# Performance work log

Hardware: AMD Instinct MI355X
Metric: run time of the kernel (lower is better)

## Reference

```python
import jax, jax.numpy as jnp
import numpy as np

B, T, D, H = 2, 2048, 1024, 16
DH = D // H

def setup_inputs() -> dict:
    key = jax.random.key(0)
    ks = jax.random.split(key, 5)
    scale = 1.0 / np.sqrt(D)
    x = jax.random.normal(ks[0], (B, T, D), dtype=jnp.float32)
    Wq = jax.random.normal(ks[1], (D, D), dtype=jnp.float32) * scale
    Wk = jax.random.normal(ks[2], (D, D), dtype=jnp.float32) * scale
    Wv = jax.random.normal(ks[3], (D, D), dtype=jnp.float32) * scale
    Wo = jax.random.normal(ks[4], (D, D), dtype=jnp.float32) * scale
    # causal mask: True means masked (matches torch masked_fill semantics)
    mask = jnp.triu(jnp.ones((T, T), dtype=bool), k=1)
    return {"x": x, "mask": mask, "Wq": Wq, "Wk": Wk, "Wv": Wv, "Wo": Wo}

def reference(x, mask, Wq, Wk, Wv, Wo):
    b, t, c = x.shape
    # projections -> [B, H, T, DH]
    def split_heads(y):
        return y.reshape(b, t, H, DH).transpose(0, 2, 1, 3)
    q = split_heads(x @ Wq)
    k = split_heads(x @ Wk)
    v = split_heads(x @ Wv)
    # scores [B, H, T, T]
    att = jnp.einsum('bhqd,bhkd->bhqk', q, k) / jnp.sqrt(jnp.float32(DH))
    att = jnp.where(mask, -jnp.inf, att)
    att = jax.nn.softmax(att, axis=-1)
    # dropout=0.0 (eval-mode determinism)
    out = jnp.einsum('bhqk,bhkd->bhqd', att, v)
    out = out.transpose(0, 2, 1, 3).reshape(b, t, c)
    return out @ Wo
```

## Files before the change

kernel.cpp:

```cpp
#include <hip/hip_runtime.h>
#include <stdint.h>

typedef unsigned short u16;
typedef unsigned int u32;
typedef __attribute__((ext_vector_type(8))) short s16x8;
typedef __attribute__((ext_vector_type(4))) float f32x4;
typedef __attribute__((ext_vector_type(8))) unsigned short u16x8;
typedef __attribute__((ext_vector_type(4))) unsigned short u16x4;

#define T_ 2048
#define D_ 1024
#define H_ 16
#define DH_ 64

#define QSCALE_LOG2E 0.18033688011112042f

#if __has_builtin(__builtin_amdgcn_exp2f)
#define EXP2(x) __builtin_amdgcn_exp2f(x)
#else
#define EXP2(x) exp2f(x)
#endif

__device__ __forceinline__ float bf2f(u16 u) {
    union { unsigned int i; float f; } x; x.i = ((unsigned int)u) << 16; return x.f;
}
__device__ __forceinline__ u16 f2bf(float f) {
    union { float f; unsigned int i; } x; x.f = f;
    unsigned int u = x.i;
    u += 0x7fffu + ((u >> 16) & 1u);
    return (u16)(u >> 16);
}
__device__ __forceinline__ u32 pack_rn(float a, float b) {
    union { float f; u32 u; } ua, ub; ua.f = a; ub.f = b;
    return ((ua.u + 0x8000u) >> 16) | ((ub.u + 0x8000u) & 0xffff0000u);
}

__device__ __forceinline__ void gload16(const u16* g, u16* l) {
    __builtin_amdgcn_global_load_lds(
        (const __attribute__((address_space(1))) void*)g,
        (__attribute__((address_space(3))) void*)l,
        16, 0, 0);
}

__global__ __launch_bounds__(256) void prep_kernel(const float* __restrict__ x,
                                                   const float* __restrict__ Wq,
                                                   const float* __restrict__ Wk,
                                                   const float* __restrict__ Wv,
                                                   const float* __restrict__ Wo,
                                                   u16* __restrict__ xb,
                                                   u16* __restrict__ WT) {
    __shared__ float tile[32][33];
    int blk = blockIdx.x;
    if (blk < 4096) {
        int i = (blk * 256 + threadIdx.x) * 4;
        float4 v = *(const float4*)(x + i);
        u16x4 o;
        o[0] = f2bf(v.x); o[1] = f2bf(v.y); o[2] = f2bf(v.z); o[3] = f2bf(v.w);
        *(u16x4*)(xb + i) = o;
    } else {
        int t = blk - 4096;
        int s = t >> 10;
        const float* W = (s == 0) ? Wq : (s == 1) ? Wk : (s == 2) ? Wv : Wo;
        int n0 = ((t >> 5) & 31) * 32;
        int k0 = (t & 31) * 32;
        int tx = threadIdx.x & 31, ty = threadIdx.x >> 5;
        #pragma unroll
        for (int j = 0; j < 32; j += 8)
            tile[ty + j][tx] = W[(k0 + ty + j) * D_ + n0 + tx];
        __syncthreads();
        u16* dst = WT + (size_t)s * D_ * D_;
        #pragma unroll
        for (int j = 0; j < 32; j += 8)
            dst[(n0 + ty + j) * D_ + k0 + tx] = f2bf(tile[tx][ty + j]);
    }
}

__global__ __launch_bounds__(256) void gemm_qkv(const u16* __restrict__ A,
                                                const u16* __restrict__ Bt,
                                                u16* __restrict__ Qw,
                                                u16* __restrict__ Kw,
                                                u16* __restrict__ Vw) {
    __shared__ __align__(16) u16 As[2][128 * 32];
    __shared__ __align__(16) u16 Bs[2][128 * 32];
    const int m0 = blockIdx.x * 128, n0 = blockIdx.y * 128;
    int tid = threadIdx.x;
    int w = tid >> 6, lane = tid & 63, quad = lane >> 4, l15 = lane & 15;
    int wr = w >> 1, wc = w & 1;

    int nb0 = (w << 7), nb1 = nb0 + 64;
    int c0 = nb0 + lane, c1 = nb1 + lane;
    int r0 = c0 >> 2, k0off = (((c0 & 3) ^ ((r0 >> 1) & 3)) << 3);
    int r1 = c1 >> 2, k1off = (((c1 & 3) ^ ((r1 >> 1) & 3)) << 3);
    const u16* Ar0 = A + (size_t)(m0 + r0) * D_ + k0off;
    const u16* Ar1 = A + (size_t)(m0 + r1) * D_ + k1off;
    const u16* Br0 = Bt + (size_t)(n0 + r0) * D_ + k0off;
    const u16* Br1 = Bt + (size_t)(n0 + r1) * D_ + k1off;

    f32x4 acc[4][4];
    #pragma unroll
    for (int mi = 0; mi < 4; ++mi)
        #pragma unroll
        for (int ni = 0; ni < 4; ++ni) acc[mi][ni] = (f32x4){0.f, 0.f, 0.f, 0.f};

    gload16(Ar0, &As[0][nb0 << 3]);
    gload16(Ar1, &As[0][nb1 << 3]);
    gload16(Br0, &Bs[0][nb0 << 3]);
    gload16(Br1, &Bs[0][nb1 << 3]);

    for (int k0 = 0; k0 < D_; k0 += 32) {
        int buf = (k0 >> 5) & 1;
        __syncthreads();
        if (k0 + 32 < D_) {
            int kn = k0 + 32;
            gload16(Ar0 + kn, &As[buf ^ 1][nb0 << 3]);
            gload16(Ar1 + kn, &As[buf ^ 1][nb1 << 3]);
            gload16(Br0 + kn, &Bs[buf ^ 1][nb0 << 3]);
            gload16(Br1 + kn, &Bs[buf ^ 1][nb1 << 3]);
        }
        s16x8 af[4], bf[4];
        #pragma unroll
        for (int mi = 0; mi < 4; ++mi) {
            int R = wr * 64 + mi * 16 + l15;
            af[mi] = *(const s16x8*)&As[buf][((R << 2) | (quad ^ ((R >> 1) & 3))) << 3];
        }
        #pragma unroll
        for (int ni = 0; ni < 4; ++ni) {
            int R = wc * 64 + ni * 16 + l15;
            bf[ni] = *(const s16x8*)&Bs[buf][((R << 2) | (quad ^ ((R >> 1) & 3))) << 3];
        }
        #pragma unroll
        for (int mi = 0; mi < 4; ++mi)
            #pragma unroll
            for (int ni = 0; ni < 4; ++ni)
                acc[mi][ni] = __builtin_amdgcn_mfma_f32_16x16x32_bf16(af[mi], bf[ni],
                                                                      acc[mi][ni], 0, 0, 0);
    }

    #pragma unroll
    for (int mi = 0; mi < 4; ++mi) {
        int mbase = m0 + wr * 64 + mi * 16 + quad * 4;
        #pragma unroll
        for (int ni = 0; ni < 4; ++ni) {
            int n = n0 + wc * 64 + ni * 16 + l15;
            int b = mbase >> 11, t0 = mbase & 2047;
            int sel = n >> 10, nn = n & 1023;
            int h = nn >> 6, dh = nn & 63;
            int bhidx = (b << 4) + h;
            if (sel == 0) {
                #pragma unroll
                for (int r = 0; r < 4; ++r)
                    Qw[(size_t)(bhidx * T_ + t0 + r) * DH_ + dh] =
                        f2bf(acc[mi][ni][r] * QSCALE_LOG2E);
            } else if (sel == 1) {
                #pragma unroll
                for (int r = 0; r < 4; ++r)
                    Kw[(size_t)(bhidx * T_ + t0 + r) * DH_ + dh] = f2bf(acc[mi][ni][r]);
            } else {
                uint2 pk;
                pk.x = pack_rn(acc[mi][ni][0], acc[mi][ni][1]);
                pk.y = pack_rn(acc[mi][ni][2], acc[mi][ni][3]);
                *(uint2*)(Vw + ((size_t)bhidx * DH_ + dh) * T_ + t0) = pk;
            }
        }
    }
}

__global__ __launch_bounds__(256) void gemm_out(const u16* __restrict__ A,
                                                const u16* __restrict__ Bt,
                                                float* __restrict__ Cout) {
    __shared__ __align__(16) u16 As[2][128 * 32];
    __shared__ __align__(16) u16 Bs[2][64 * 32];
    const int m0 = blockIdx.x * 128, n0 = blockIdx.y * 64;
    int tid = threadIdx.x;
    int w = tid >> 6, lane = tid & 63, quad = lane >> 4, l15 = lane & 15;

    int nbA0 = (w << 7), nbA1 = nbA0 + 64, nbB = (w << 6);
    int cA0 = nbA0 + lane, cA1 = nbA1 + lane, cB = nbB + lane;
    int rA0 = cA0 >> 2, kA0 = (((cA0 & 3) ^ ((rA0 >> 1) & 3)) << 3);
    int rA1 = cA1 >> 2, kA1 = (((cA1 & 3) ^ ((rA1 >> 1) & 3)) << 3);
    int rB  = cB >> 2,  kB  = (((cB  & 3) ^ ((rB  >> 1) & 3)) << 3);
    const u16* ArA0 = A + (size_t)(m0 + rA0) * D_ + kA0;
    const u16* ArA1 = A + (size_t)(m0 + rA1) * D_ + kA1;
    const u16* BrB  = Bt + (size_t)(n0 + rB) * D_ + kB;

    f32x4 acc[2][4];
    #pragma unroll
    for (int mi = 0; mi < 2; ++mi)
        #pragma unroll
        for (int ni = 0; ni < 4; ++ni) acc[mi][ni] = (f32x4){0.f, 0.f, 0.f, 0.f};

    gload16(ArA0, &As[0][nbA0 << 3]);
    gload16(ArA1, &As[0][nbA1 << 3]);
    gload16(BrB,  &Bs[0][nbB << 3]);

    for (int k0 = 0; k0 < D_; k0 += 32) {
        int buf = (k0 >> 5) & 1;
        __syncthreads();
        if (k0 + 32 < D_) {
            int kn = k0 + 32;
            gload16(ArA0 + kn, &As[buf ^ 1][nbA0 << 3]);
            gload16(ArA1 + kn, &As[buf ^ 1][nbA1 << 3]);
            gload16(BrB + kn,  &Bs[buf ^ 1][nbB << 3]);
        }
        s16x8 af[2], bf[4];
        #pragma unroll
        for (int mi = 0; mi < 2; ++mi) {
            int R = w * 32 + mi * 16 + l15;
            af[mi] = *(const s16x8*)&As[buf][((R << 2) | (quad ^ ((R >> 1) & 3))) << 3];
        }
        #pragma unroll
        for (int ni = 0; ni < 4; ++ni) {
            int R = ni * 16 + l15;
            bf[ni] = *(const s16x8*)&Bs[buf][((R << 2) | (quad ^ ((R >> 1) & 3))) << 3];
        }
        #pragma unroll
        for (int mi = 0; mi < 2; ++mi)
            #pragma unroll
            for (int ni = 0; ni < 4; ++ni)
                acc[mi][ni] = __builtin_amdgcn_mfma_f32_16x16x32_bf16(af[mi], bf[ni],
                                                                      acc[mi][ni], 0, 0, 0);
    }

    #pragma unroll
    for (int mi = 0; mi < 2; ++mi) {
        int mbase = m0 + w * 32 + mi * 16 + quad * 4;
        #pragma unroll
        for (int ni = 0; ni < 4; ++ni) {
            int n = n0 + ni * 16 + l15;
            #pragma unroll
            for (int r = 0; r < 4; ++r)
                Cout[(size_t)(mbase + r) * D_ + n] = acc[mi][ni][r];
        }
    }
}

__global__ __launch_bounds__(256) void attn_mfma_kernel(const u16* __restrict__ Qg,
                                                        const u16* __restrict__ Kg,
                                                        const u16* __restrict__ Vt,
                                                        u16* __restrict__ Opart,
                                                        float* __restrict__ lpart) {
    __shared__ __align__(16) u16 Kbuf[2][64 * 64];
    __shared__ __align__(16) u16 Vbuf[2][64 * 64];
    __shared__ __align__(16) u16 Ps[4][2][16][72];

    int blk = blockIdx.x;
    int xcd = blk & 7, slot = blk >> 3;
    int bh = (xcd << 2) + (slot / 40);
    int x  = slot % 40;
    int BX, c;
    if (x < 4)       { BX = x;                    c = 0; }
    else if (x < 12) { BX = 4 + ((x - 4) >> 1);   c = (x - 4) & 1; }
    else if (x < 24) { BX = 8 + (x - 12) / 3;     c = (x - 12) % 3; }
    else             { BX = 12 + ((x - 24) >> 2); c = (x - 24) & 3; }
    int kstart = c << 3;
    int ktm = 2 * BX + 1;
    int kend = min(kstart + 8, ktm + 1);

    int tid = threadIdx.x;
    int w = tid >> 6, lane = tid & 63, quad = lane >> 4, l15 = lane & 15;
    int q0 = BX << 7;
    int qA = q0 + 16 * w;
    int qB = q0 + 64 + 16 * w;

    const u16* Qb = Qg + (size_t)bh * T_ * DH_;
    const u16* Kb = Kg + (size_t)bh * T_ * DH_;
    const u16* Vb = Vt + (size_t)bh * DH_ * T_;

    s16x8 qa0 = *(const s16x8*)(Qb + (size_t)(qA + l15) * DH_ + quad * 8);
    s16x8 qa1 = *(const s16x8*)(Qb + (size_t)(qA + l15) * DH_ + quad * 8 + 32);
    s16x8 qc0 = *(const s16x8*)(Qb + (size_t)(qB + l15) * DH_ + quad * 8);
    s16x8 qc1 = *(const s16x8*)(Qb + (size_t)(qB + l15) * DH_ + quad * 8 + 32);

    int nb0 = (w << 7), nb1 = nb0 + 64;
    int n0c = nb0 + lane, n1c = nb1 + lane;
    int r0 = n0c >> 3, c0s = n0c & 7, g0 = (r0 << 3) + (c0s ^ (r0 & 7));
    int r1 = n1c >> 3, c1s = n1c & 7, g1 = (r1 << 3) + (c1s ^ (r1 & 7));

    {
        int kb0 = kstart << 6;
        const u16* Ktile = Kb + (size_t)kb0 * DH_;
        gload16(Ktile + (g0 << 3), &Kbuf[0][nb0 << 3]);
        gload16(Ktile + (g1 << 3), &Kbuf[0][nb1 << 3]);
        gload16(Vb + (size_t)r0 * T_ + kb0 + ((g0 & 7) << 3), &Vbuf[0][nb0 << 3]);
        gload16(Vb + (size_t)r1 * T_ + kb0 + ((g1 & 7) << 3), &Vbuf[0][nb1 << 3]);
    }

    f32x4 oA[4] = {{0.f,0.f,0.f,0.f},{0.f,0.f,0.f,0.f},{0.f,0.f,0.f,0.f},{0.f,0.f,0.f,0.f}};
    f32x4 oB[4] = {{0.f,0.f,0.f,0.f},{0.f,0.f,0.f,0.f},{0.f,0.f,0.f,0.f},{0.f,0.f,0.f,0.f}};
    float lA = 0.f, lB = 0.f;

    for (int kt = kstart; kt < kend; ++kt) {
        int buf = (kt - kstart) & 1;
        __syncthreads();

        if (kt + 1 < kend) {
            int kb2 = (kt + 1) << 6;
            const u16* Ktile = Kb + (size_t)kb2 * DH_;
            gload16(Ktile + (g0 << 3), &Kbuf[buf ^ 1][nb0 << 3]);
            gload16(Ktile + (g1 << 3), &Kbuf[buf ^ 1][nb1 << 3]);
            gload16(Vb + (size_t)r0 * T_ + kb2 + ((g0 & 7) << 3), &Vbuf[buf ^ 1][nb0 << 3]);
            gload16(Vb + (size_t)r1 * T_ + kb2 + ((g1 & 7) << 3), &Vbuf[buf ^ 1][nb1 << 3]);
        }

        f32x4 sA[4], sB[4];
        #pragma unroll
        for (int g = 0; g < 4; ++g) {
            int r = (g << 4) + l15;
            int cc = quad ^ (r & 7);
            s16x8 ka0 = *(const s16x8*)&Kbuf[buf][((r << 3) + cc) << 3];
            s16x8 ka1 = *(const s16x8*)&Kbuf[buf][((r << 3) + (cc ^ 4)) << 3];
            f32x4 z = {0.f, 0.f, 0.f, 0.f};
            sA[g] = __builtin_amdgcn_mfma_f32_16x16x32_bf16(ka0, qa0, z, 0, 0, 0);
            sA[g] = __builtin_amdgcn_mfma_f32_16x16x32_bf16(ka1, qa1, sA[g], 0, 0, 0);
            sB[g] = __builtin_amdgcn_mfma_f32_16x16x32_bf16(ka0, qc0, z, 0, 0, 0);
            sB[g] = __builtin_amdgcn_mfma_f32_16x16x32_bf16(ka1, qc1, sB[g], 0, 0, 0);
        }

        if (kt >= ktm - 1) {
            int rA = q0 + 16 * w + l15 - (kt << 6);
            #pragma unroll
            for (int g = 0; g < 4; ++g)
                #pragma unroll
                for (int r = 0; r < 4; ++r)
                    if ((g << 4) + (quad << 2) + r > rA) sA[g][r] = -INFINITY;
        }
        if (kt == ktm) {
            int rB = 16 * w + l15;
            #pragma unroll
            for (int g = 0; g < 4; ++g)
                #pragma unroll
                for (int r = 0; r < 4; ++r)
                    if ((g << 4) + (quad << 2) + r > rB) sB[g][r] = -INFINITY;
        }

        #pragma unroll
        for (int g = 0; g < 4; ++g)
            #pragma unroll
            for (int r = 0; r < 4; ++r) {
                float pA = EXP2(sA[g][r]); sA[g][r] = pA; lA += pA;
                float pB = EXP2(sB[g][r]); sB[g][r] = pB; lB += pB;
            }

        #pragma unroll
        for (int g = 0; g < 4; ++g) {
            uint2 pkA, pkB;
            pkA.x = pack_rn(sA[g][0], sA[g][1]); pkA.y = pack_rn(sA[g][2], sA[g][3]);
            pkB.x = pack_rn(sB[g][0], sB[g][1]); pkB.y = pack_rn(sB[g][2], sB[g][3]);
            *(uint2*)&Ps[w][0][l15][g * 16 + quad * 4] = pkA;
            *(uint2*)&Ps[w][1][l15][g * 16 + quad * 4] = pkB;
        }
        s16x8 pa0 = *(const s16x8*)&Ps[w][0][l15][quad * 8];
        s16x8 pa1 = *(const s16x8*)&Ps[w][0][l15][quad * 8 + 32];
        s16x8 pc0 = *(const s16x8*)&Ps[w][1][l15][quad * 8];
        s16x8 pc1 = *(const s16x8*)&Ps[w][1][l15][quad * 8 + 32];

        #pragma unroll
        for (int g = 0; g < 4; ++g) {
            int r = (g << 4) + l15;
            int cc = quad ^ (r & 7);
            s16x8 va0 = *(const s16x8*)&Vbuf[buf][((r << 3) + cc) << 3];
            s16x8 va1 = *(const s16x8*)&Vbuf[buf][((r << 3) + (cc ^ 4)) << 3];
            oA[g] = __builtin_amdgcn_mfma_f32_16x16x32_bf16(va0, pa0, oA[g], 0, 0, 0);
            oA[g] = __builtin_amdgcn_mfma_f32_16x16x32_bf16(va1, pa1, oA[g], 0, 0, 0);
            oB[g] = __builtin_amdgcn_mfma_f32_16x16x32_bf16(va0, pc0, oB[g], 0, 0, 0);
            oB[g] = __builtin_amdgcn_mfma_f32_16x16x32_bf16(va1, pc1, oB[g], 0, 0, 0);
        }
    }

    lA += __shfl_xor(lA, 16); lA += __shfl_xor(lA, 32);
    lB += __shfl_xor(lB, 16); lB += __shfl_xor(lB, 32);
    int slotid = ((bh << 4) + BX) * 4 + c;
    u16* dA = Opart + ((size_t)slotid * 128 + 16 * w + l15) * 64;
    u16* dB = dA + 64 * 64;
    #pragma unroll
    for (int g = 0; g < 4; ++g) {
        uint2 pk;
        pk.x = pack_rn(oA[g][0], oA[g][1]); pk.y = pack_rn(oA[g][2], oA[g][3]);
        *(uint2*)(dA + (g << 4) + (quad << 2)) = pk;
        pk.x = pack_rn(oB[g][0], oB[g][1]); pk.y = pack_rn(oB[g][2], oB[g][3]);
        *(uint2*)(dB + (g << 4) + (quad << 2)) = pk;
    }
    if (quad == 0) {
        lpart[(size_t)slotid * 128 + 16 * w + l15] = lA;
        lpart[(size_t)slotid * 128 + 64 + 16 * w + l15] = lB;
    }
}

__global__ __launch_bounds__(256) void reduce_attn(const u16* __restrict__ Opart,
                                                   const float* __restrict__ lpart,
                                                   u16* __restrict__ att) {
    int BX = blockIdx.x, bh = blockIdx.y;
    int nch = (BX >> 2) + 1;
    int tid = threadIdx.x;
    int row = tid >> 1, dh0 = (tid & 1) << 5;
    int slotbase = ((bh << 4) + BX) << 2;

    float acc[32];
    #pragma unroll
    for (int i = 0; i < 32; ++i) acc[i] = 0.f;
    float l = 0.f;
    for (int cc = 0; cc < nch; ++cc) {
        const u16* op = Opart + ((size_t)(slotbase + cc) * 128 + row) * 64 + dh0;
        #pragma unroll
        for (int v = 0; v < 4; ++v) {
            u16x8 o8 = *(const u16x8*)(op + v * 8);
            #pragma unroll
            for (int j = 0; j < 8; ++j) acc[v * 8 + j] += bf2f(o8[j]);
        }
        l += lpart[(size_t)(slotbase + cc) * 128 + row];
    }
    float inv = 1.f / l;
    int b = bh >> 4, h = bh & 15;
    int q = (BX << 7) + row;
    u16* dst = att + ((size_t)(b * T_) + q) * D_ + (h << 6) + dh0;
    #pragma unroll
    for (int v = 0; v < 4; ++v) {
        u16x8 o8;
        #pragma unroll
        for (int j = 0; j < 8; ++j) o8[j] = f2bf(acc[v * 8 + j] * inv);
        *(u16x8*)(dst + v * 8) = o8;
    }
}

extern "C" void kernel_launch(void* const* d_in, const int* in_sizes, int n_in,
                              void* d_out, int out_size, void* d_ws, size_t ws_size,
                              hipStream_t stream) {
    const float* x  = (const float*)d_in[0];
    const float* Wq = (const float*)d_in[2];
    const float* Wk = (const float*)d_in[3];
    const float* Wv = (const float*)d_in[4];
    const float* Wo = (const float*)d_in[5];
    float* out = (float*)d_out;

    char* ws = (char*)d_ws;
    u16*   xb    = (u16*)(ws);
    u16*   WT    = (u16*)(ws + (8ull  << 20));
    u16*   Qw    = (u16*)(ws + (16ull << 20));
    u16*   Kw    = (u16*)(ws + (24ull << 20));
    u16*   Vw    = (u16*)(ws + (32ull << 20));
    u16*   att   = (u16*)(ws + (40ull << 20));
    u16*   Opart = (u16*)(ws + (48ull << 20));
    float* lpart = (float*)(ws + (82ull << 20));

    prep_kernel<<<dim3(8192), dim3(256), 0, stream>>>(x, Wq, Wk, Wv, Wo, xb, WT);
    gemm_qkv<<<dim3(32, 24), dim3(256), 0, stream>>>(xb, WT, Qw, Kw, Vw);
    attn_mfma_kernel<<<dim3(1280), dim3(256), 0, stream>>>(Qw, Kw, Vw, Opart, lpart);
    reduce_attn<<<dim3(16, 32), dim3(256), 0, stream>>>(Opart, lpart, att);
    gemm_out<<<dim3(32, 16), dim3(256), 0, stream>>>(att, WT + 3ull * 1048576ull, out);
}
```

Measured before the change: 194.5 us.

## Build P fragments in registers via permlane swaps; rebalance causal K-chunk split

The bf16 P operand for the PV MFMA is now built in registers with v_cvt_pk_bf16_f32 and permlane16/32 swaps, replacing the round trip through the Ps shared buffer. This removes LDS stores and loads and frees shared memory, and the kernel now declares launch bounds with 4 blocks per SM. K-tile ranges are spread evenly across the chunks of each query block instead of fixed 8-tile chunks, which evens out per-block work. The row sums use two accumulators to shorten the dependency chain. The packing of the output partials also switches to the hardware convert instruction, which may round slightly differently from the previous manual rounding.

```diff
diff --git a/kernel.cpp b/kernel.cpp
--- a/kernel.cpp
+++ b/kernel.cpp
@@ -33,6 +33,33 @@
 __device__ __forceinline__ u32 pack_rn(float a, float b) {
     union { float f; u32 u; } ua, ub; ua.f = a; ub.f = b;
     return ((ua.u + 0x8000u) >> 16) | ((ub.u + 0x8000u) & 0xffff0000u);
+}
+__device__ __forceinline__ u32 cvtpk(float lo, float hi) {
+    u32 r;
+    asm("v_cvt_pk_bf16_f32 %0, %1, %2" : "=v"(r) : "v"(lo), "v"(hi));
+    return r;
+}
+__device__ __forceinline__ void plswap32(u32 &a, u32 &b) {
+    asm("v_permlane32_swap_b32 %0, %1" : "+v"(a), "+v"(b));
+}
+__device__ __forceinline__ void plswap16(u32 &a, u32 &b) {
+    asm("v_permlane16_swap_b32 %0, %1" : "+v"(a), "+v"(b));
+}
+__device__ __forceinline__ s16x8 frag4(u32 a, u32 b, u32 c, u32 d) {
+    union { u32 u[4]; s16x8 v; } x;
+    x.u[0] = a; x.u[1] = b; x.u[2] = c; x.u[3] = d; return x.v;
+}
+__device__ __forceinline__ void p_frags(const f32x4 s[4], s16x8 &p0, s16x8 &p1) {
+    u32 w00 = cvtpk(s[0][0], s[0][1]), w01 = cvtpk(s[0][2], s[0][3]);
+    u32 w10 = cvtpk(s[1][0], s[1][1]), w11 = cvtpk(s[1][2], s[1][3]);
+    u32 w20 = cvtpk(s[2][0], s[2][1]), w21 = cvtpk(s[2][2], s[2][3]);
+    u32 w30 = cvtpk(s[3][0], s[3][1]), w31 = cvtpk(s[3][2], s[3][3]);
+    plswap32(w00, w10); plswap16(w00, w10);
+    plswap32(w01, w11); plswap16(w01, w11);
+    plswap32(w20, w30); plswap16(w20, w30);
+    plswap32(w21, w31); plswap16(w21, w31);
+    p0 = frag4(w00, w01, w10, w11);
+    p1 = frag4(w20, w21, w30, w31);
 }
 
 __device__ __forceinline__ void gload16(const u16* g, u16* l) {
@@ -234,14 +261,13 @@
     }
 }
 
-__global__ __launch_bounds__(256) void attn_mfma_kernel(const u16* __restrict__ Qg,
-                                                        const u16* __restrict__ Kg,
-                                                        const u16* __restrict__ Vt,
-                                                        u16* __restrict__ Opart,
-                                                        float* __restrict__ lpart) {
+__global__ __launch_bounds__(256, 4) void attn_mfma_kernel(const u16* __restrict__ Qg,
+                                                           const u16* __restrict__ Kg,
+                                                           const u16* __restrict__ Vt,
+                                                           u16* __restrict__ Opart,
+                                                           float* __restrict__ lpart) {
     __shared__ __align__(16) u16 Kbuf[2][64 * 64];
     __shared__ __align__(16) u16 Vbuf[2][64 * 64];
-    __shared__ __align__(16) u16 Ps[4][2][16][72];
 
     int blk = blockIdx.x;
     int xcd = blk & 7, slot = blk >> 3;
@@ -252,9 +278,12 @@
     else if (x < 12) { BX = 4 + ((x - 4) >> 1);   c = (x - 4) & 1; }
     else if (x < 24) { BX = 8 + (x - 12) / 3;     c = (x - 12) % 3; }
     else             { BX = 12 + ((x - 24) >> 2); c = (x - 24) & 3; }
-    int kstart = c << 3;
     int ktm = 2 * BX + 1;
-    int kend = min(kstart + 8, ktm + 1);
+    int ntile = ktm + 1;
+    int nch = (BX >> 2) + 1;
+    int base = ntile / nch, rem = ntile % nch;
+    int kstart = c * base + (c < rem ? c : rem);
+    int kend = kstart + base + (c < rem ? 1 : 0);
 
     int tid = threadIdx.x;
     int w = tid >> 6, lane = tid & 63, quad = lane >> 4, l15 = lane & 15;
@@ -288,6 +317,7 @@
     f32x4 oA[4] = {{0.f,0.f,0.f,0.f},{0.f,0.f,0.f,0.f},{0.f,0.f,0.f,0.f},{0.f,0.f,0.f,0.f}};
     f32x4 oB[4] = {{0.f,0.f,0.f,0.f},{0.f,0.f,0.f,0.f},{0.f,0.f,0.f,0.f},{0.f,0.f,0.f,0.f}};
     float lA = 0.f, lB = 0.f;
+    float lA1 = 0.f, lB1 = 0.f;
 
     for (int kt = kstart; kt < kend; ++kt) {
         int buf = (kt - kstart) & 1;
@@ -334,25 +364,20 @@
         }
 
         #pragma unroll
-        for (int g = 0; g < 4; ++g)
-            #pragma unroll
-            for (int r = 0; r < 4; ++r) {
-                float pA = EXP2(sA[g][r]); sA[g][r] = pA; lA += pA;
-                float pB = EXP2(sB[g][r]); sB[g][r] = pB; lB += pB;
-            }
-
-        #pragma unroll
         for (int g = 0; g < 4; ++g) {
-            uint2 pkA, pkB;
-            pkA.x = pack_rn(sA[g][0], sA[g][1]); pkA.y = pack_rn(sA[g][2], sA[g][3]);
-            pkB.x = pack_rn(sB[g][0], sB[g][1]); pkB.y = pack_rn(sB[g][2], sB[g][3]);
-            *(uint2*)&Ps[w][0][l15][g * 16 + quad * 4] = pkA;
-            *(uint2*)&Ps[w][1][l15][g * 16 + quad * 4] = pkB;
-        }
-        s16x8 pa0 = *(const s16x8*)&Ps[w][0][l15][quad * 8];
-        s16x8 pa1 = *(const s16x8*)&Ps[w][0][l15][quad * 8 + 32];
-        s16x8 pc0 = *(const s16x8*)&Ps[w][1][l15][quad * 8];
-        s16x8 pc1 = *(const s16x8*)&Ps[w][1][l15][quad * 8 + 32];
+            float pA0 = EXP2(sA[g][0]); sA[g][0] = pA0; lA  += pA0;
+            float pA1 = EXP2(sA[g][1]); sA[g][1] = pA1; lA1 += pA1;
+            float pA2 = EXP2(sA[g][2]); sA[g][2] = pA2; lA  += pA2;
+            float pA3 = EXP2(sA[g][3]); sA[g][3] = pA3; lA1 += pA3;
+            float pB0 = EXP2(sB[g][0]); sB[g][0] = pB0; lB  += pB0;
+            float pB1 = EXP2(sB[g][1]); sB[g][1] = pB1; lB1 += pB1;
+            float pB2 = EXP2(sB[g][2]); sB[g][2] = pB2; lB  += pB2;
+            float pB3 = EXP2(sB[g][3]); sB[g][3] = pB3; lB1 += pB3;
+        }
+
+        s16x8 pa0, pa1, pc0, pc1;
+        p_frags(sA, pa0, pa1);
+        p_frags(sB, pc0, pc1);
 
         #pragma unroll
         for (int g = 0; g < 4; ++g) {
@@ -367,6 +392,7 @@
         }
     }
 
+    lA += lA1; lB += lB1;
     lA += __shfl_xor(lA, 16); lA += __shfl_xor(lA, 32);
     lB += __shfl_xor(lB, 16); lB += __shfl_xor(lB, 32);
     int slotid = ((bh << 4) + BX) * 4 + c;
@@ -375,9 +401,9 @@
     #pragma unroll
     for (int g = 0; g < 4; ++g) {
         uint2 pk;
-        pk.x = pack_rn(oA[g][0], oA[g][1]); pk.y = pack_rn(oA[g][2], oA[g][3]);
+        pk.x = cvtpk(oA[g][0], oA[g][1]); pk.y = cvtpk(oA[g][2], oA[g][3]);
         *(uint2*)(dA + (g << 4) + (quad << 2)) = pk;
-        pk.x = pack_rn(oB[g][0], oB[g][1]); pk.y = pack_rn(oB[g][2], oB[g][3]);
+        pk.x = cvtpk(oB[g][0], oB[g][1]); pk.y = cvtpk(oB[g][2], oB[g][3]);
         *(uint2*)(dB + (g << 4) + (quad << 2)) = pk;
     }
     if (quad == 0) {
```

New measurement: 187.2 us. 1.04x faster.
